# Kernel optimization log

Measured on AMD Instinct MI355X. Metric: run time of the kernel, lower is better.

The kernel has to match this reference:

```python
import jax, jax.numpy as jnp
import numpy as np
from jax.scipy.special import logsumexp

T, N, M = 131072, 64, 8  # T_max, n_states, m_dimensions


def setup_inputs() -> dict:
    key = jax.random.key(0)
    k1, k2, k3, k4 = jax.random.split(key, 4)
    # observed Poisson counts, shape (T, M)
    x = jax.random.randint(k1, (T, M), 0, 20, dtype=jnp.int32)
    # Poisson rates per state/dimension (positive), shape (N, M)
    lambdas = jnp.exp(jax.random.uniform(k2, (N, M), dtype=jnp.float32) * 3.0)
    # column-stochastic transition matrix in log domain (softmax over dim 0, as in torch code)
    log_transition = jax.nn.log_softmax(
        jax.random.uniform(k3, (N, N), dtype=jnp.float32) * 10.0, axis=0)
    # log state priors, shape (N,)
    log_state_priors = jax.nn.log_softmax(
        jax.random.normal(k4, (N,), dtype=jnp.float32), axis=0)
    return {"x": x, "lambdas": lambdas, "log_transition": log_transition,
            "log_state_priors": log_state_priors}


def reference(x, lambdas, log_transition, log_state_priors):
    """log p(x) for a Poisson-emission HMM (forward algorithm in log domain)."""
    xf = x.astype(jnp.float32)                      # (T, M)
    log_lam = jnp.log(lambdas)                      # (N, M)
    # Poisson log-prob summed over dims: em[t,s] = sum_m x[t,m]*log lam[s,m] - lam[s,m] - lgamma(x[t,m]+1)
    log_em = (xf @ log_lam.T                        # (T, N)
              - lambdas.sum(axis=1)[None, :]
              - jax.lax.lgamma(xf + 1.0).sum(axis=1)[:, None])

    alpha0 = log_em[0] + log_state_priors           # (N,)

    def step(alpha_prev, em_t):
        # alpha[t,i] = em[t,i] + logsumexp_k (A[i,k] + alpha[t-1,k])
        alpha = em_t + logsumexp(log_transition + alpha_prev[None, :], axis=1)
        return alpha, None

    alpha_T, _ = jax.lax.scan(step, alpha0, log_em[1:])
    return logsumexp(alpha_T)
```

## Files before the change

kernel.cpp:

```cpp
#include <hip/hip_runtime.h>
#include <stdint.h>

#define TT 131072
#define MD 8
#define CHUNK 32
#define NCH 1024
#define RMP 72

using f32x4  = __attribute__((ext_vector_type(4))) float;
using bf16x8 = __attribute__((ext_vector_type(8))) __bf16;
using bf16x2 = __attribute__((ext_vector_type(2))) __bf16;
using u32x2  = __attribute__((ext_vector_type(2))) uint32_t;
using u32x4  = __attribute__((ext_vector_type(4))) uint32_t;

__device__ __constant__ float c_lg[20] = {
    0.0f, 0.0f, 0.69314718f, 1.79175947f, 3.17805383f,
    4.78749174f, 6.57925121f, 8.52516136f, 10.60460290f, 12.80182748f,
    15.10441257f, 17.50230785f, 19.98721386f, 22.55216385f, 25.19122118f,
    27.89927138f, 30.67186011f, 33.50507345f, 36.39544521f, 39.33988419f};

#define MFMA(a, b, c) __builtin_amdgcn_mfma_f32_16x16x32_bf16((a), (b), (c), 0, 0, 0)

__device__ __forceinline__ uint32_t pk2(float lo, float hi) {
    bf16x2 t = {(__bf16)lo, (__bf16)hi};
    return __builtin_bit_cast(uint32_t, t);
}

__device__ __forceinline__ float wave_max_dpp(float v) {
    int x = __builtin_bit_cast(int, v);
#define DHOP(ctrl)                                                            \
    {                                                                         \
        int y = __builtin_amdgcn_update_dpp(x, x, ctrl, 0xf, 0xf, false);     \
        x = __builtin_bit_cast(int, fmaxf(__builtin_bit_cast(float, x),       \
                                          __builtin_bit_cast(float, y)));     \
    }
    DHOP(0x111)
    DHOP(0x112)
    DHOP(0x114)
    DHOP(0x118)
    DHOP(0x142)
    DHOP(0x143)
#undef DHOP
    return __builtin_bit_cast(float, __builtin_amdgcn_readlane(x, 63));
}


__device__ __forceinline__ void emis(const int4& xa, const int4& xb,
                                     const float* ll, float lamsum,
                                     const float* lgt, float& pe, float& gs) {
    float g = -lamsum;
    g = fmaf((float)xa.x, ll[0], g);
    g = fmaf((float)xa.y, ll[1], g);
    g = fmaf((float)xa.z, ll[2], g);
    g = fmaf((float)xa.w, ll[3], g);
    g = fmaf((float)xb.x, ll[4], g);
    g = fmaf((float)xb.y, ll[5], g);
    g = fmaf((float)xb.z, ll[6], g);
    g = fmaf((float)xb.w, ll[7], g);
    float Lt = lgt[xa.x] + lgt[xa.y] + lgt[xa.z] + lgt[xa.w] +
               lgt[xb.x] + lgt[xb.y] + lgt[xb.z] + lgt[xb.w];
    float gm = wave_max_dpp(g);
    pe = __expf(g - gm);
    gs = gm - Lt;
}

__device__ __forceinline__ void emis_ng(const int4& xa, const int4& xb,
                                        const float* ll, float lamsum,
                                        float& pe, float& gm_out) {
    float g = -lamsum;
    g = fmaf((float)xa.x, ll[0], g);
    g = fmaf((float)xa.y, ll[1], g);
    g = fmaf((float)xa.z, ll[2], g);
    g = fmaf((float)xa.w, ll[3], g);
    g = fmaf((float)xb.x, ll[4], g);
    g = fmaf((float)xb.y, ll[5], g);
    g = fmaf((float)xb.z, ll[6], g);
    g = fmaf((float)xb.w, ll[7], g);
    float gm = wave_max_dpp(g);
    pe = __expf(g - gm);
    gm_out = gm;
}


__device__ __forceinline__ void identity_B(bf16x8 B[2][4], int li, int q) {
#pragma unroll
    for (int kf = 0; kf < 2; ++kf)
#pragma unroll
        for (int nb = 0; nb < 4; ++nb) {
            int n = 16 * nb + li;
            u32x4 u;
#pragma unroll
            for (int wi = 0; wi < 4; ++wi) {
                int k0 = 32 * kf + 16 * (wi >> 1) + 4 * q + 2 * (wi & 1);
                uint32_t v = 0;
                if (k0 == n) v |= 0x3F80u;
                if (k0 + 1 == n) v |= 0x3F800000u;
                u[wi] = v;
            }
            B[kf][nb] = __builtin_bit_cast(bf16x8, u);
        }
}

__device__ __forceinline__ void state_to_rm(short* rm, const bf16x8 B[2][4],
                                            int li, int q) {
#pragma unroll
    for (int kf = 0; kf < 2; ++kf)
#pragma unroll
        for (int nb = 0; nb < 4; ++nb) {
            u32x4 u = __builtin_bit_cast(u32x4, B[kf][nb]);
            int n = 16 * nb + li;
#pragma unroll
            for (int wi = 0; wi < 4; ++wi) {
                int k0 = 32 * kf + 16 * (wi >> 1) + 4 * q + 2 * (wi & 1);
                uint32_t v = u[wi];
                rm[k0 * RMP + n] = (short)(v & 0xFFFFu);
                rm[(k0 + 1) * RMP + n] = (short)(v >> 16);
            }
        }
}

__device__ __forceinline__ void dump_rm_g(short* gm, const bf16x8 B[2][4],
                                          int li, int q) {
#pragma unroll
    for (int kf = 0; kf < 2; ++kf)
#pragma unroll
        for (int nb = 0; nb < 4; ++nb) {
            u32x4 u = __builtin_bit_cast(u32x4, B[kf][nb]);
            int n = 16 * nb + li;
#pragma unroll
            for (int wi = 0; wi < 4; ++wi) {
                int k0 = 32 * kf + 16 * (wi >> 1) + 4 * q + 2 * (wi & 1);
                uint32_t v = u[wi];
                gm[k0 * 64 + n] = (short)(v & 0xFFFFu);
                gm[(k0 + 1) * 64 + n] = (short)(v >> 16);
            }
        }
}

__device__ __forceinline__ void load_afrags(const short* rm, int li, int q,
                                            bf16x8 A[4][2]) {
#pragma unroll
    for (int mb = 0; mb < 4; ++mb)
#pragma unroll
        for (int kf = 0; kf < 2; ++kf) {
            const short* p = rm + (16 * mb + li) * RMP + 32 * kf + 4 * q;
            u32x2 lo = *(const u32x2*)p;
            u32x2 hi = *(const u32x2*)(p + 16);
            u32x4 u = {lo[0], lo[1], hi[0], hi[1]};
            A[mb][kf] = __builtin_bit_cast(bf16x8, u);
        }
}

__device__ __forceinline__ void load_afrags_g(const short* gm, int li, int q,
                                              bf16x8 A[4][2]) {
#pragma unroll
    for (int mb = 0; mb < 4; ++mb)
#pragma unroll
        for (int kf = 0; kf < 2; ++kf) {
            const short* p = gm + (16 * mb + li) * 64 + 32 * kf + 4 * q;
            u32x2 lo = *(const u32x2*)p;
            u32x2 hi = *(const u32x2*)(p + 16);
            u32x4 u = {lo[0], lo[1], hi[0], hi[1]};
            A[mb][kf] = __builtin_bit_cast(bf16x8, u);
        }
}

__device__ __forceinline__ float leftmul(const bf16x8 A[4][2], bf16x8 B[2][4]) {
    f32x4 d[4][4];
#pragma unroll
    for (int mb = 0; mb < 4; ++mb)
#pragma unroll
        for (int nb = 0; nb < 4; ++nb) {
            f32x4 z = {0.f, 0.f, 0.f, 0.f};
            d[mb][nb] = MFMA(A[mb][0], B[0][nb], z);
            d[mb][nb] = MFMA(A[mb][1], B[1][nb], d[mb][nb]);
        }
    float pm = 0.f;
#pragma unroll
    for (int mb = 0; mb < 4; ++mb)
#pragma unroll
        for (int nb = 0; nb < 4; ++nb)
            pm = fmaxf(pm, fmaxf(fmaxf(d[mb][nb][0], d[mb][nb][1]),
                                 fmaxf(d[mb][nb][2], d[mb][nb][3])));
    pm = wave_max_dpp(pm);
    pm = fmaxf(pm, 1e-30f);
    float r = 1.0f / pm;
#pragma unroll
    for (int mb = 0; mb < 4; ++mb)
#pragma unroll
        for (int nb = 0; nb < 4; ++nb) {
#pragma unroll
            for (int reg = 0; reg < 4; ++reg)
                B[mb >> 1][nb][(mb & 1) * 4 + reg] =
                    (__bf16)(d[mb][nb][reg] * r);
        }
    return pm;
}

#define STEP(BIN, BOUT, RS, WS, NRMV, GSC, GSN)                              \
    {                                                                        \
        int tn = t0 + s + 2;                                                 \
        tn = tn > TT - 1 ? TT - 1 : tn;                                      \
        int4 xan = *(const int4*)(x + (size_t)tn * MD);                      \
        int4 xbn = *(const int4*)(x + (size_t)tn * MD + 4);                  \
        float pe_n, gm_n;                                                    \
        emis_ng(xa1, xb1, ll, lamsum, pe_n, gm_n);                           \
        GSN = gm_n;                                                          \
        pes[WS][w][l] = pe_n;                                                \
        float r = 1.0f / NRMV;                                               \
        S += (double)GSC + (double)__logf(NRMV);                             \
        const float* pc = &pes[RS][w][0];                                    \
        f32x4 scv0 = *(const f32x4*)(pc + 4 * q) * r;                        \
        f32x4 scv1 = *(const f32x4*)(pc + 16 + 4 * q) * r;                   \
        f32x4 scv2 = *(const f32x4*)(pc + 32 + 4 * q) * r;                   \
        f32x4 scv3 = *(const f32x4*)(pc + 48 + 4 * q) * r;                   \
        f32x4 mx = {0.f, 0.f, 0.f, 0.f};                                     \
        _Pragma("unroll") for (int nb = 0; nb < 4; ++nb) {                   \
            f32x4 z = {0.f, 0.f, 0.f, 0.f};                                  \
            f32x4 d0 = MFMA(TA[0][0], BIN[0][nb], z);                        \
            d0 = MFMA(TA[0][1], BIN[1][nb], d0);                             \
            f32x4 d1 = MFMA(TA[1][0], BIN[0][nb], z);                        \
            d1 = MFMA(TA[1][1], BIN[1][nb], d1);                             \
            d0 *= scv0;                                                      \
            d1 *= scv1;                                                      \
            mx = __builtin_elementwise_max(mx, d0);                          \
            mx = __builtin_elementwise_max(mx, d1);                          \
            u32x4 u0 = {pk2(d0[0], d0[1]), pk2(d0[2], d0[3]),                \
                        pk2(d1[0], d1[1]), pk2(d1[2], d1[3])};               \
            BOUT[0][nb] = __builtin_bit_cast(bf16x8, u0);                    \
            f32x4 d2 = MFMA(TA[2][0], BIN[0][nb], z);                        \
            d2 = MFMA(TA[2][1], BIN[1][nb], d2);                             \
            f32x4 d3 = MFMA(TA[3][0], BIN[0][nb], z);                        \
            d3 = MFMA(TA[3][1], BIN[1][nb], d3);                             \
            d2 *= scv2;                                                      \
            d3 *= scv3;                                                      \
            mx = __builtin_elementwise_max(mx, d2);                          \
            mx = __builtin_elementwise_max(mx, d3);                          \
            u32x4 u1 = {pk2(d2[0], d2[1]), pk2(d2[2], d2[3]),                \
                        pk2(d3[0], d3[1]), pk2(d3[2], d3[3])};               \
            BOUT[1][nb] = __builtin_bit_cast(bf16x8, u1);                    \
        }                                                                    \
        float pm = fmaxf(fmaxf(mx[0], mx[1]), fmaxf(mx[2], mx[3]));          \
        pm = wave_max_dpp(pm);                                               \
        NRMV = fmaxf(pm, 1e-30f);                                            \
        xa1 = xan;                                                           \
        xb1 = xbn;                                                           \
        ++s;                                                                 \
    }

__global__ __launch_bounds__(256, 3) void k_chunks(
    const int* __restrict__ x, const float* __restrict__ lambdas,
    const float* __restrict__ logT, short* __restrict__ M1,
    double* __restrict__ S1) {
    __shared__ short rm[3][64 * RMP];
    __shared__ float pes[2][4][64];
    __shared__ float lgt[20];
    __shared__ double Sw[4];
    const int tid = threadIdx.x;
    const int l = tid & 63, w = tid >> 6;
    const int li = l & 15, q = l >> 4;
    if (tid < 20) lgt[tid] = c_lg[tid];

    float ll[8];
    float lamsum = 0.f;
#pragma unroll
    for (int m = 0; m < 8; ++m) {
        float lam = lambdas[l * 8 + m];
        ll[m] = __logf(lam);
        lamsum += lam;
    }

    bf16x8 TA[4][2];
#pragma unroll
    for (int mb = 0; mb < 4; ++mb)
#pragma unroll
        for (int kf = 0; kf < 2; ++kf) {
            const float* tp = logT + (16 * mb + li) * 64 + 32 * kf + 4 * q;
            float4 v0 = *(const float4*)tp;
            float4 v1 = *(const float4*)(tp + 16);
            bf16x8 a;
            a[0] = (__bf16)__expf(v0.x);
            a[1] = (__bf16)__expf(v0.y);
            a[2] = (__bf16)__expf(v0.z);
            a[3] = (__bf16)__expf(v0.w);
            a[4] = (__bf16)__expf(v1.x);
            a[5] = (__bf16)__expf(v1.y);
            a[6] = (__bf16)__expf(v1.z);
            a[7] = (__bf16)__expf(v1.w);
            TA[mb][kf] = a;
        }

    bf16x8 B0[2][4], B1[2][4];
    identity_B(B0, li, q);
    __syncthreads();

    const int c = blockIdx.x * 4 + w;
    const int t0 = 1 + c * CHUNK;
    const int len = min(CHUNK, TT - t0);

    double S = 0.0;
    float nA = 1.0f, nBv = 1.0f;
    float gsA = 0.f, gsB = 0.f;
    int4 xa1, xb1;
    {
        int4 xa0 = *(const int4*)(x + (size_t)t0 * MD);
        int4 xb0 = *(const int4*)(x + (size_t)t0 * MD + 4);
        int t1 = t0 + 1 > TT - 1 ? TT - 1 : t0 + 1;
        xa1 = *(const int4*)(x + (size_t)t1 * MD);
        xb1 = *(const int4*)(x + (size_t)t1 * MD + 4);
        float pe0;
        emis_ng(xa0, xb0, ll, lamsum, pe0, gsA);
        pes[0][w][l] = pe0;
    }

    int s = 0;
    const int np = len >> 1;
#pragma unroll 1
    for (int p = 0; p < np; ++p) {
        STEP(B0, B1, 0, 1, nA, gsA, gsB);
        STEP(B1, B0, 1, 0, nBv, gsB, gsA);
    }
    if (len & 1) {
        STEP(B0, B1, 0, 1, nA, gsA, gsB);
#pragma unroll
        for (int kf = 0; kf < 2; ++kf)
#pragma unroll
            for (int nb = 0; nb < 4; ++nb) B0[kf][nb] = B1[kf][nb];
    }

    {
        float lt = 0.f;
        if (l < len) {
            const int4* xp = (const int4*)(x + (size_t)(t0 + l) * MD);
            int4 a = xp[0], b = xp[1];
            lt = lgt[a.x] + lgt[a.y] + lgt[a.z] + lgt[a.w] + lgt[b.x] +
                 lgt[b.y] + lgt[b.z] + lgt[b.w];
        }
#pragma unroll
        for (int m = 1; m <= 32; m <<= 1) lt += __shfl_xor(lt, m, 64);
        S -= (double)lt;
    }

    if (w) state_to_rm(&rm[w - 1][0], B0, li, q);
    if (l == 0) Sw[w] = S;
    __syncthreads();
    if (w == 0) {
#pragma unroll 1
        for (int j = 1; j < 4; ++j) {
            bf16x8 A[4][2];
            load_afrags(&rm[j - 1][0], li, q, A);
            float pm = leftmul(A, B0);
            S += Sw[j] + (double)__logf(pm);
        }
        dump_rm_g(M1 + (size_t)blockIdx.x * 4096, B0, li, q);
        if (l == 0) S1[blockIdx.x] = S;
    }
}

__global__ __launch_bounds__(256, 1) void k_combine(
    const short* __restrict__ M1, const double* __restrict__ S1,
    short* __restrict__ M2, double* __restrict__ S2) {
    __shared__ short rm[3][64 * RMP];
    __shared__ double Sw[4];
    const int tid = threadIdx.x;
    const int l = tid & 63, w = tid >> 6;
    const int li = l & 15, q = l >> 4;
    const int base = (blockIdx.x * 4 + w) * 8;

    bf16x8 B[2][4];
    identity_B(B, li, q);
    double S = 0.0;
    bf16x8 Aa[4][2], Ab[4][2];
    load_afrags_g(M1 + (size_t)base * 4096, li, q, Aa);
#pragma unroll
    for (int j = 0; j < 8; j += 2) {
        load_afrags_g(M1 + (size_t)(base + j + 1) * 4096, li, q, Ab);
        float pm = leftmul(Aa, B);
        S += S1[base + j] + (double)__logf(pm);
        if (j + 2 < 8)
            load_afrags_g(M1 + (size_t)(base + j + 2) * 4096, li, q, Aa);
        pm = leftmul(Ab, B);
        S += S1[base + j + 1] + (double)__logf(pm);
    }

    if (w) state_to_rm(&rm[w - 1][0], B, li, q);
    if (l == 0) Sw[w] = S;
    __syncthreads();
    if (w == 0) {
#pragma unroll 1
        for (int j = 1; j < 4; ++j) {
            bf16x8 A[4][2];
            load_afrags(&rm[j - 1][0], li, q, A);
            float pm = leftmul(A, B);
            S += Sw[j] + (double)__logf(pm);
        }
        dump_rm_g(M2 + (size_t)blockIdx.x * 4096, B, li, q);
        if (l == 0) S2[blockIdx.x] = S;
    }
}

__global__ __launch_bounds__(256, 1) void k_final(
    const int* __restrict__ x, const float* __restrict__ lambdas,
    const float* __restrict__ prior, const short* __restrict__ M2,
    const double* __restrict__ S2, float* __restrict__ out) {
    __shared__ short rm[3][64 * RMP];
    __shared__ double Sw[4];
    __shared__ float lgt[20];
    const int tid = threadIdx.x;
    const int l = tid & 63, w = tid >> 6;
    const int li = l & 15, q = l >> 4;
    if (tid < 20) lgt[tid] = c_lg[tid];
    __syncthreads();

    const int base = w * 8;
    bf16x8 B[2][4];
    identity_B(B, li, q);
    double S = 0.0;
    bf16x8 Aa[4][2], Ab[4][2];
    load_afrags_g(M2 + (size_t)base * 4096, li, q, Aa);
#pragma unroll
    for (int j = 0; j < 8; j += 2) {
        load_afrags_g(M2 + (size_t)(base + j + 1) * 4096, li, q, Ab);
        float pm = leftmul(Aa, B);
        S += S2[base + j] + (double)__logf(pm);
        if (j + 2 < 8)
            load_afrags_g(M2 + (size_t)(base + j + 2) * 4096, li, q, Aa);
        pm = leftmul(Ab, B);
        S += S2[base + j + 1] + (double)__logf(pm);
    }

    if (w) state_to_rm(&rm[w - 1][0], B, li, q);
    if (l == 0) Sw[w] = S;
    __syncthreads();
    if (w == 0) {
#pragma unroll 1
        for (int j = 1; j < 4; ++j) {
            bf16x8 A[4][2];
            load_afrags(&rm[j - 1][0], li, q, A);
            float pm = leftmul(A, B);
            S += Sw[j] + (double)__logf(pm);
        }
        float ll[8];
        float lamsum = 0.f;
#pragma unroll
        for (int m = 0; m < 8; ++m) {
            float lam = lambdas[l * 8 + m];
            ll[m] = __logf(lam);
            lamsum += lam;
        }
        int4 xa = *(const int4*)(x);
        int4 xb = *(const int4*)(x + 4);
        float pe0, gs0;
        emis(xa, xb, ll, lamsum, lgt, pe0, gs0);
        S += (double)gs0;
        float a0 = pe0 * __expf(prior[l]);

        float av[4];
#pragma unroll
        for (int nb = 0; nb < 4; ++nb) av[nb] = __shfl(a0, 16 * nb + li, 64);

        float acc = 0.f;
#pragma unroll
        for (int kf = 0; kf < 2; ++kf)
#pragma unroll
            for (int nb = 0; nb < 4; ++nb) {
                u32x4 u = __builtin_bit_cast(u32x4, B[kf][nb]);
#pragma unroll
                for (int e = 0; e < 4; ++e) {
                    float flo = __builtin_bit_cast(float, u[e] << 16);
                    float fhi = __builtin_bit_cast(float, u[e] & 0xFFFF0000u);
                    acc = fmaf(flo + fhi, av[nb], acc);
                }
            }
#pragma unroll
        for (int m = 1; m <= 32; m <<= 1) acc += __shfl_xor(acc, m, 64);
        if (l == 0) out[0] = (float)(S + (double)__logf(acc));
    }
}

extern "C" void kernel_launch(void* const* d_in, const int* in_sizes, int n_in,
                              void* d_out, int out_size, void* d_ws,
                              size_t ws_size, hipStream_t stream) {
    const int* x = (const int*)d_in[0];
    const float* lambdas = (const float*)d_in[1];
    const float* logT = (const float*)d_in[2];
    const float* prior = (const float*)d_in[3];
    float* out = (float*)d_out;
    char* ws = (char*)d_ws;
    short* M1 = (short*)ws;
    double* S1 = (double*)(ws + 8388608);
    short* M2 = (short*)(ws + 8396800);
    double* S2 = (double*)(ws + 8658944);

    k_chunks<<<NCH, 256, 0, stream>>>(x, lambdas, logT, M1, S1);
    k_combine<<<32, 256, 0, stream>>>(M1, S1, M2, S2);
    k_final<<<1, 256, 0, stream>>>(x, lambdas, prior, M2, S2, out);
}
```

Baseline: 136.1 us.

## Interleave two independent chunk recurrences per wave and normalize every other step

```diff
diff --git a/kernel.cpp b/kernel.cpp
--- a/kernel.cpp
+++ b/kernel.cpp
@@ -4,7 +4,6 @@
 #define TT 131072
 #define MD 8
 #define CHUNK 32
-#define NCH 1024
 #define RMP 72
 
 using f32x4  = __attribute__((ext_vector_type(4))) float;
@@ -197,24 +196,24 @@
     return pm;
 }
 
-#define STEP(BIN, BOUT, RS, WS, NRMV, GSC, GSN)                              \
+#define STEPE(BIN, BOUT, XA1, XB1, NRM, GSC, GSN, SACC, TBASE, CHI)          \
     {                                                                        \
-        int tn = t0 + s + 2;                                                 \
-        tn = tn > TT - 1 ? TT - 1 : tn;                                      \
-        int4 xan = *(const int4*)(x + (size_t)tn * MD);                      \
-        int4 xbn = *(const int4*)(x + (size_t)tn * MD + 4);                  \
-        float pe_n, gm_n;                                                    \
-        emis_ng(xa1, xb1, ll, lamsum, pe_n, gm_n);                           \
-        GSN = gm_n;                                                          \
-        pes[WS][w][l] = pe_n;                                                \
-        float r = 1.0f / NRMV;                                               \
-        S += (double)GSC + (double)__logf(NRMV);                             \
-        const float* pc = &pes[RS][w][0];                                    \
-        f32x4 scv0 = *(const f32x4*)(pc + 4 * q) * r;                        \
-        f32x4 scv1 = *(const f32x4*)(pc + 16 + 4 * q) * r;                   \
-        f32x4 scv2 = *(const f32x4*)(pc + 32 + 4 * q) * r;                   \
-        f32x4 scv3 = *(const f32x4*)(pc + 48 + 4 * q) * r;                   \
-        f32x4 mx = {0.f, 0.f, 0.f, 0.f};                                     \
+        int tn_ = TBASE + s + 2;                                             \
+        tn_ = tn_ > TT - 1 ? TT - 1 : tn_;                                   \
+        int4 xan_ = *(const int4*)(x + (size_t)tn_ * MD);                    \
+        int4 xbn_ = *(const int4*)(x + (size_t)tn_ * MD + 4);                \
+        float pen_, gmn_;                                                    \
+        emis_ng(XA1, XB1, ll, lamsum, pen_, gmn_);                           \
+        GSN = gmn_;                                                          \
+        pes[(s + 1) & 1][CHI][w][l] = pen_;                                  \
+        float r_ = 1.0f / NRM;                                               \
+        SACC += (double)GSC + (double)__logf(NRM);                           \
+        const float* pc_ = &pes[s & 1][CHI][w][0];                           \
+        f32x4 scv0 = *(const f32x4*)(pc_ + 4 * q) * r_;                      \
+        f32x4 scv1 = *(const f32x4*)(pc_ + 16 + 4 * q) * r_;                 \
+        f32x4 scv2 = *(const f32x4*)(pc_ + 32 + 4 * q) * r_;                 \
+        f32x4 scv3 = *(const f32x4*)(pc_ + 48 + 4 * q) * r_;                 \
+        f32x4 mx_ = {0.f, 0.f, 0.f, 0.f};                                    \
         _Pragma("unroll") for (int nb = 0; nb < 4; ++nb) {                   \
             f32x4 z = {0.f, 0.f, 0.f, 0.f};                                  \
             f32x4 d0 = MFMA(TA[0][0], BIN[0][nb], z);                        \
@@ -223,8 +222,8 @@
             d1 = MFMA(TA[1][1], BIN[1][nb], d1);                             \
             d0 *= scv0;                                                      \
             d1 *= scv1;                                                      \
-            mx = __builtin_elementwise_max(mx, d0);                          \
-            mx = __builtin_elementwise_max(mx, d1);                          \
+            mx_ = __builtin_elementwise_max(mx_, d0);                        \
+            mx_ = __builtin_elementwise_max(mx_, d1);                        \
             u32x4 u0 = {pk2(d0[0], d0[1]), pk2(d0[2], d0[3]),                \
                         pk2(d1[0], d1[1]), pk2(d1[2], d1[3])};               \
             BOUT[0][nb] = __builtin_bit_cast(bf16x8, u0);                    \
@@ -234,26 +233,66 @@
             d3 = MFMA(TA[3][1], BIN[1][nb], d3);                             \
             d2 *= scv2;                                                      \
             d3 *= scv3;                                                      \
-            mx = __builtin_elementwise_max(mx, d2);                          \
-            mx = __builtin_elementwise_max(mx, d3);                          \
+            mx_ = __builtin_elementwise_max(mx_, d2);                        \
+            mx_ = __builtin_elementwise_max(mx_, d3);                        \
             u32x4 u1 = {pk2(d2[0], d2[1]), pk2(d2[2], d2[3]),                \
                         pk2(d3[0], d3[1]), pk2(d3[2], d3[3])};               \
             BOUT[1][nb] = __builtin_bit_cast(bf16x8, u1);                    \
         }                                                                    \
-        float pm = fmaxf(fmaxf(mx[0], mx[1]), fmaxf(mx[2], mx[3]));          \
-        pm = wave_max_dpp(pm);                                               \
-        NRMV = fmaxf(pm, 1e-30f);                                            \
-        xa1 = xan;                                                           \
-        xb1 = xbn;                                                           \
-        ++s;                                                                 \
-    }
-
-__global__ __launch_bounds__(256, 3) void k_chunks(
+        float pm_ = fmaxf(fmaxf(mx_[0], mx_[1]), fmaxf(mx_[2], mx_[3]));     \
+        pm_ = wave_max_dpp(pm_);                                             \
+        NRM = fmaxf(pm_, 1e-30f);                                            \
+        XA1 = xan_;                                                          \
+        XB1 = xbn_;                                                          \
+    }
+
+#define STEPO(BIN, BOUT, XA1, XB1, GSC, GSN, SACC, TBASE, CHI)               \
+    {                                                                        \
+        int tn_ = TBASE + s + 2;                                             \
+        tn_ = tn_ > TT - 1 ? TT - 1 : tn_;                                   \
+        int4 xan_ = *(const int4*)(x + (size_t)tn_ * MD);                    \
+        int4 xbn_ = *(const int4*)(x + (size_t)tn_ * MD + 4);                \
+        float pen_, gmn_;                                                    \
+        emis_ng(XA1, XB1, ll, lamsum, pen_, gmn_);                           \
+        GSN = gmn_;                                                          \
+        pes[(s + 1) & 1][CHI][w][l] = pen_;                                  \
+        SACC += (double)GSC;                                                 \
+        const float* pc_ = &pes[s & 1][CHI][w][0];                           \
+        f32x4 scv0 = *(const f32x4*)(pc_ + 4 * q);                           \
+        f32x4 scv1 = *(const f32x4*)(pc_ + 16 + 4 * q);                      \
+        f32x4 scv2 = *(const f32x4*)(pc_ + 32 + 4 * q);                      \
+        f32x4 scv3 = *(const f32x4*)(pc_ + 48 + 4 * q);                      \
+        _Pragma("unroll") for (int nb = 0; nb < 4; ++nb) {                   \
+            f32x4 z = {0.f, 0.f, 0.f, 0.f};                                  \
+            f32x4 d0 = MFMA(TA[0][0], BIN[0][nb], z);                        \
+            d0 = MFMA(TA[0][1], BIN[1][nb], d0);                             \
+            f32x4 d1 = MFMA(TA[1][0], BIN[0][nb], z);                        \
+            d1 = MFMA(TA[1][1], BIN[1][nb], d1);                             \
+            d0 *= scv0;                                                      \
+            d1 *= scv1;                                                      \
+            u32x4 u0 = {pk2(d0[0], d0[1]), pk2(d0[2], d0[3]),                \
+                        pk2(d1[0], d1[1]), pk2(d1[2], d1[3])};               \
+            BOUT[0][nb] = __builtin_bit_cast(bf16x8, u0);                    \
+            f32x4 d2 = MFMA(TA[2][0], BIN[0][nb], z);                        \
+            d2 = MFMA(TA[2][1], BIN[1][nb], d2);                             \
+            f32x4 d3 = MFMA(TA[3][0], BIN[0][nb], z);                        \
+            d3 = MFMA(TA[3][1], BIN[1][nb], d3);                             \
+            d2 *= scv2;                                                      \
+            d3 *= scv3;                                                      \
+            u32x4 u1 = {pk2(d2[0], d2[1]), pk2(d2[2], d2[3]),                \
+                        pk2(d3[0], d3[1]), pk2(d3[2], d3[3])};               \
+            BOUT[1][nb] = __builtin_bit_cast(bf16x8, u1);                    \
+        }                                                                    \
+        XA1 = xan_;                                                          \
+        XB1 = xbn_;                                                          \
+    }
+
+__global__ __launch_bounds__(256, 2) void k_chunks(
     const int* __restrict__ x, const float* __restrict__ lambdas,
     const float* __restrict__ logT, short* __restrict__ M1,
     double* __restrict__ S1) {
-    __shared__ short rm[3][64 * RMP];
-    __shared__ float pes[2][4][64];
+    __shared__ short rm[4][64 * RMP];
+    __shared__ float pes[2][2][4][64];
     __shared__ float lgt[20];
     __shared__ double Sw[4];
     const int tid = threadIdx.x;
@@ -290,109 +329,137 @@
             TA[mb][kf] = a;
         }
 
-    bf16x8 B0[2][4], B1[2][4];
-    identity_B(B0, li, q);
+    bf16x8 B0a[2][4], B1a[2][4], B0b[2][4], B1b[2][4];
+    identity_B(B0a, li, q);
+    identity_B(B0b, li, q);
     __syncthreads();
 
-    const int c = blockIdx.x * 4 + w;
-    const int t0 = 1 + c * CHUNK;
-    const int len = min(CHUNK, TT - t0);
-
-    double S = 0.0;
-    float nA = 1.0f, nBv = 1.0f;
-    float gsA = 0.f, gsB = 0.f;
-    int4 xa1, xb1;
+    const int c0 = (blockIdx.x * 4 + w) * 2;
+    const int t0a = 1 + c0 * CHUNK;
+    const int t0b = t0a + CHUNK;
+    const int lenB = min(CHUNK, TT - t0b);
+
+    double Sa = 0.0, Sb = 0.0;
+    float nA_a = 1.0f, nA_b = 1.0f;
+    float gsAa = 0.f, gsBa = 0.f, gsAb = 0.f, gsBb = 0.f;
+    int4 xa1a, xb1a, xa1b, xb1b;
     {
-        int4 xa0 = *(const int4*)(x + (size_t)t0 * MD);
-        int4 xb0 = *(const int4*)(x + (size_t)t0 * MD + 4);
-        int t1 = t0 + 1 > TT - 1 ? TT - 1 : t0 + 1;
-        xa1 = *(const int4*)(x + (size_t)t1 * MD);
-        xb1 = *(const int4*)(x + (size_t)t1 * MD + 4);
+        int4 x0 = *(const int4*)(x + (size_t)t0a * MD);
+        int4 x1 = *(const int4*)(x + (size_t)t0a * MD + 4);
         float pe0;
-        emis_ng(xa0, xb0, ll, lamsum, pe0, gsA);
-        pes[0][w][l] = pe0;
+        emis_ng(x0, x1, ll, lamsum, pe0, gsAa);
+        pes[0][0][w][l] = pe0;
+        xa1a = *(const int4*)(x + (size_t)(t0a + 1) * MD);
+        xb1a = *(const int4*)(x + (size_t)(t0a + 1) * MD + 4);
+        int4 y0 = *(const int4*)(x + (size_t)t0b * MD);
+        int4 y1 = *(const int4*)(x + (size_t)t0b * MD + 4);
+        emis_ng(y0, y1, ll, lamsum, pe0, gsAb);
+        pes[0][1][w][l] = pe0;
+        int t1b = t0b + 1 > TT - 1 ? TT - 1 : t0b + 1;
+        xa1b = *(const int4*)(x + (size_t)t1b * MD);
+        xb1b = *(const int4*)(x + (size_t)t1b * MD + 4);
     }
 
     int s = 0;
-    const int np = len >> 1;
 #pragma unroll 1
-    for (int p = 0; p < np; ++p) {
-        STEP(B0, B1, 0, 1, nA, gsA, gsB);
-        STEP(B1, B0, 1, 0, nBv, gsB, gsA);
-    }
-    if (len & 1) {
-        STEP(B0, B1, 0, 1, nA, gsA, gsB);
+    for (int p = 0; p < 15; ++p) {
+        STEPE(B0a, B1a, xa1a, xb1a, nA_a, gsAa, gsBa, Sa, t0a, 0);
+        STEPE(B0b, B1b, xa1b, xb1b, nA_b, gsAb, gsBb, Sb, t0b, 1);
+        ++s;
+        STEPO(B1a, B0a, xa1a, xb1a, gsBa, gsAa, Sa, t0a, 0);
+        STEPO(B1b, B0b, xa1b, xb1b, gsBb, gsAb, Sb, t0b, 1);
+        ++s;
+    }
+    STEPE(B0a, B1a, xa1a, xb1a, nA_a, gsAa, gsBa, Sa, t0a, 0);
+    STEPE(B0b, B1b, xa1b, xb1b, nA_b, gsAb, gsBb, Sb, t0b, 1);
+    ++s;
+    STEPO(B1a, B0a, xa1a, xb1a, gsBa, gsAa, Sa, t0a, 0);
+    if (lenB == CHUNK) {
+        STEPO(B1b, B0b, xa1b, xb1b, gsBb, gsAb, Sb, t0b, 1);
+    } else {
 #pragma unroll
         for (int kf = 0; kf < 2; ++kf)
 #pragma unroll
-            for (int nb = 0; nb < 4; ++nb) B0[kf][nb] = B1[kf][nb];
+            for (int nb = 0; nb < 4; ++nb) B0b[kf][nb] = B1b[kf][nb];
     }
 
     {
+        const int lenTot = CHUNK + lenB;
         float lt = 0.f;
-        if (l < len) {
-            const int4* xp = (const int4*)(x + (size_t)(t0 + l) * MD);
+        if (l < lenTot) {
+            const int4* xp = (const int4*)(x + (size_t)(t0a + l) * MD);
             int4 a = xp[0], b = xp[1];
             lt = lgt[a.x] + lgt[a.y] + lgt[a.z] + lgt[a.w] + lgt[b.x] +
                  lgt[b.y] + lgt[b.z] + lgt[b.w];
         }
 #pragma unroll
         for (int m = 1; m <= 32; m <<= 1) lt += __shfl_xor(lt, m, 64);
-        S -= (double)lt;
-    }
-
-    if (w) state_to_rm(&rm[w - 1][0], B0, li, q);
+        Sa -= (double)lt;
+    }
+
+    state_to_rm(&rm[w][0], B0b, li, q);
+    {
+        bf16x8 Ap[4][2];
+        load_afrags(&rm[w][0], li, q, Ap);
+        float pm = leftmul(Ap, B0a);
+        Sa += Sb + (double)__logf(pm);
+    }
+
+    __syncthreads();
+    if (w) state_to_rm(&rm[w][0], B0a, li, q);
+    if (l == 0) Sw[w] = Sa;
+    __syncthreads();
+    if (w == 0) {
+        double S = Sa;
+#pragma unroll 1
+        for (int j = 1; j < 4; ++j) {
+            bf16x8 A[4][2];
+            load_afrags(&rm[j][0], li, q, A);
+            float pm = leftmul(A, B0a);
+            S += Sw[j] + (double)__logf(pm);
+        }
+        dump_rm_g(M1 + (size_t)blockIdx.x * 4096, B0a, li, q);
+        if (l == 0) S1[blockIdx.x] = S;
+    }
+}
+
+__global__ __launch_bounds__(256, 1) void k_combine(
+    const short* __restrict__ M1, const double* __restrict__ S1,
+    short* __restrict__ M2, double* __restrict__ S2) {
+    __shared__ short rm[4][64 * RMP];
+    __shared__ double Sw[4];
+    const int tid = threadIdx.x;
+    const int l = tid & 63, w = tid >> 6;
+    const int li = l & 15, q = l >> 4;
+    const int base = (blockIdx.x * 4 + w) * 4;
+
+    bf16x8 B[2][4];
+    identity_B(B, li, q);
+    double S = 0.0;
+    bf16x8 Aa[4][2], Ab[4][2];
+    load_afrags_g(M1 + (size_t)base * 4096, li, q, Aa);
+    load_afrags_g(M1 + (size_t)(base + 1) * 4096, li, q, Ab);
+    float pm = leftmul(Aa, B);
+    S += S1[base] + (double)__logf(pm);
+    load_afrags_g(M1 + (size_t)(base + 2) * 4096, li, q, Aa);
+    pm = leftmul(Ab, B);
+    S += S1[base + 1] + (double)__logf(pm);
+    load_afrags_g(M1 + (size_t)(base + 3) * 4096, li, q, Ab);
+    pm = leftmul(Aa, B);
+    S += S1[base + 2] + (double)__logf(pm);
+    pm = leftmul(Ab, B);
+    S += S1[base + 3] + (double)__logf(pm);
+
+    if (w) state_to_rm(&rm[w][0], B, li, q);
     if (l == 0) Sw[w] = S;
     __syncthreads();
     if (w == 0) {
 #pragma unroll 1
         for (int j = 1; j < 4; ++j) {
             bf16x8 A[4][2];
-            load_afrags(&rm[j - 1][0], li, q, A);
-            float pm = leftmul(A, B0);
-            S += Sw[j] + (double)__logf(pm);
-        }
-        dump_rm_g(M1 + (size_t)blockIdx.x * 4096, B0, li, q);
-        if (l == 0) S1[blockIdx.x] = S;
-    }
-}
-
-__global__ __launch_bounds__(256, 1) void k_combine(
-    const short* __restrict__ M1, const double* __restrict__ S1,
-    short* __restrict__ M2, double* __restrict__ S2) {
-    __shared__ short rm[3][64 * RMP];
-    __shared__ double Sw[4];
-    const int tid = threadIdx.x;
-    const int l = tid & 63, w = tid >> 6;
-    const int li = l & 15, q = l >> 4;
-    const int base = (blockIdx.x * 4 + w) * 8;
-
-    bf16x8 B[2][4];
-    identity_B(B, li, q);
-    double S = 0.0;
-    bf16x8 Aa[4][2], Ab[4][2];
-    load_afrags_g(M1 + (size_t)base * 4096, li, q, Aa);
-#pragma unroll
-    for (int j = 0; j < 8; j += 2) {
-        load_afrags_g(M1 + (size_t)(base + j + 1) * 4096, li, q, Ab);
-        float pm = leftmul(Aa, B);
-        S += S1[base + j] + (double)__logf(pm);
-        if (j + 2 < 8)
-            load_afrags_g(M1 + (size_t)(base + j + 2) * 4096, li, q, Aa);
-        pm = leftmul(Ab, B);
-        S += S1[base + j + 1] + (double)__logf(pm);
-    }
-
-    if (w) state_to_rm(&rm[w - 1][0], B, li, q);
-    if (l == 0) Sw[w] = S;
-    __syncthreads();
-    if (w == 0) {
-#pragma unroll 1
-        for (int j = 1; j < 4; ++j) {
-            bf16x8 A[4][2];
-            load_afrags(&rm[j - 1][0], li, q, A);
-            float pm = leftmul(A, B);
-            S += Sw[j] + (double)__logf(pm);
+            load_afrags(&rm[j][0], li, q, A);
+            float pmj = leftmul(A, B);
+            S += Sw[j] + (double)__logf(pmj);
         }
         dump_rm_g(M2 + (size_t)blockIdx.x * 4096, B, li, q);
         if (l == 0) S2[blockIdx.x] = S;
@@ -403,7 +470,7 @@
     const int* __restrict__ x, const float* __restrict__ lambdas,
     const float* __restrict__ prior, const short* __restrict__ M2,
     const double* __restrict__ S2, float* __restrict__ out) {
-    __shared__ short rm[3][64 * RMP];
+    __shared__ short rm[4][64 * RMP];
     __shared__ double Sw[4];
     __shared__ float lgt[20];
     const int tid = threadIdx.x;
@@ -429,14 +496,14 @@
         S += S2[base + j + 1] + (double)__logf(pm);
     }
 
-    if (w) state_to_rm(&rm[w - 1][0], B, li, q);
+    if (w) state_to_rm(&rm[w][0], B, li, q);
     if (l == 0) Sw[w] = S;
     __syncthreads();
     if (w == 0) {
 #pragma unroll 1
         for (int j = 1; j < 4; ++j) {
             bf16x8 A[4][2];
-            load_afrags(&rm[j - 1][0], li, q, A);
+            load_afrags(&rm[j][0], li, q, A);
             float pm = leftmul(A, B);
             S += Sw[j] + (double)__logf(pm);
         }
@@ -488,11 +555,11 @@
     float* out = (float*)d_out;
     char* ws = (char*)d_ws;
     short* M1 = (short*)ws;
-    double* S1 = (double*)(ws + 8388608);
-    short* M2 = (short*)(ws + 8396800);
-    double* S2 = (double*)(ws + 8658944);
-
-    k_chunks<<<NCH, 256, 0, stream>>>(x, lambdas, logT, M1, S1);
+    double* S1 = (double*)(ws + 4194304);
+    short* M2 = (short*)(ws + 4198400);
+    double* S2 = (double*)(ws + 4460544);
+
+    k_chunks<<<512, 256, 0, stream>>>(x, lambdas, logT, M1, S1);
     k_combine<<<32, 256, 0, stream>>>(M1, S1, M2, S2);
     k_final<<<1, 256, 0, stream>>>(x, lambdas, prior, M2, S2, out);
 }
```

Result: faster. 118.1 us (-13.2%).
